# Kernel optimization log

Hardware: AMD Instinct MI355X
Metric: run time of the kernel (lower is better)

The kernel has to match this reference:

```python
import jax, jax.numpy as jnp
import numpy as np

B, CIN, COUT, H, W, K = 32, 256, 256, 64, 64, 3


def setup_inputs() -> dict:
    key = jax.random.key(0)
    k1, k2, k3 = jax.random.split(key, 3)
    x = jax.random.normal(k1, (B, CIN, H, W), dtype=jnp.float32)
    # kaiming_uniform_ with a=sqrt(5): bound = sqrt(6 / ((1 + a^2) * fan_in)) = sqrt(1/fan_in)
    fan_in = CIN * K * K
    bound = float(np.sqrt(1.0 / fan_in))
    weight = jax.random.uniform(k2, (COUT, CIN, K, K), dtype=jnp.float32,
                                minval=-bound, maxval=bound)
    bias = jax.random.normal(k3, (COUT,), dtype=jnp.float32)
    return {"x": x, "weight": weight, "bias": bias}


def reference(x, weight, bias):
    # CustomConvnd with kernel=3, stride=1, padding=1 (module doubles it, pad
    # helper splits around center -> 1 element each side, zero padding),
    # equivalent to a standard 2D cross-correlation like torch Conv2d.
    out = jax.lax.conv_general_dilated(
        x, weight,
        window_strides=(1, 1),
        padding=((1, 1), (1, 1)),
        dimension_numbers=("NCHW", "OIHW", "NCHW"),
    )
    return out + bias[None, :, None, None]
```

## Files before the change

### kernel.cpp

```cpp
#include <hip/hip_runtime.h>
#include <hip/hip_bf16.h>

typedef __attribute__((ext_vector_type(8))) short short8;
typedef __attribute__((ext_vector_type(16))) float floatx16;

#define BDIM 256

constexpr int kCIN = 256, kCOUT = 256, kH = 64, kW = 64;
constexpr int BK = 32;
constexpr int NCHUNK = kCIN / BK;
constexpr int ROWS = 2;
constexpr int XR = ROWS + 2, XC = 66, NPIX = XR * XC;
constexpr int HW = kH * kW;
constexpr int NSTEP = NCHUNK * 9;

constexpr int XS_PLANE = NPIX * 16;
constexpr int XS_BUF   = 4 * XS_PLANE;
constexpr int WS_PLANE = 256 * 16;
constexpr int WS_BUF   = 4 * WS_PLANE;

__device__ __forceinline__ unsigned short f2bf(float f) {
    unsigned u = __float_as_uint(f);
    u += 0x7fffu + ((u >> 16) & 1u);
    return (unsigned short)(u >> 16);
}

__global__ void wt_transform_kernel(const float* __restrict__ wsrc,
                                    unsigned short* __restrict__ wt2) {
    int idx = blockIdx.x * 256 + threadIdx.x;
    if (idx >= 9 * 256 * 256) return;
    int j  = idx & 7;
    int co = (idx >> 3) & 255;
    int g  = (idx >> 11) & 3;
    int chunk = (idx >> 13) & 7;
    int kk = idx >> 16;
    int ci = chunk * 32 + g * 8 + j;
    wt2[idx] = f2bf(wsrc[(co * 256 + ci) * 9 + kk]);
}

__global__ __launch_bounds__(BDIM, 2)
void conv3x3_mfma_kernel(const float* __restrict__ x,
                         const unsigned short* __restrict__ wt2,
                         const float* __restrict__ bias,
                         float* __restrict__ out) {
    __shared__ __align__(16) char xs[2 * XS_BUF];
    __shared__ __align__(16) char ws[2 * WS_BUF];

    const int bid = blockIdx.x;
    const int b  = bid >> 5;
    const int h0 = (bid & 31) * ROWS;

    const int tid = threadIdx.x;
    const int wv  = tid >> 6;
    const int l   = tid & 63;
    const int l31 = l & 31;
    const int hi2 = l >> 5;
    const int cog  = (wv & 1) * 128;
    const int wrow = wv >> 1;

    const float* xb = x + (size_t)b * kCIN * HW;

    floatx16 acc[4][2] = {};

    auto stageW = [&](int st) {
        int chunk = st / 9, kk = st - chunk * 9;
        char* wbuf = ws + (st & 1) * WS_BUF;
        const unsigned short* wp = wt2 + (size_t)(kk * 8 + chunk) * 8192;
        #pragma unroll
        for (int it = 0; it < 4; ++it) {
            int c = wv * 4 + it;
            int g = c >> 2;
            int row0 = (c & 3) * 64;
            const unsigned short* src = wp + (g * 256 + row0 + l) * 8;
            __builtin_amdgcn_global_load_lds(
                (const __attribute__((address_space(1))) unsigned int*)src,
                (__attribute__((address_space(3))) unsigned int*)
                    (wbuf + g * WS_PLANE + row0 * 16),
                16, 0, 0);
        }
    };

    auto stageX = [&](int chunk) {
        char* xbuf = xs + (chunk & 1) * XS_BUF;
        const int ci0 = chunk * BK;
        for (int t = tid; t < NPIX * 4; t += BDIM) {
            int g = t / NPIX;
            int rem = t - g * NPIX;
            int r = rem / XC;
            int c = rem - r * XC;
            int ih = h0 - 1 + r;
            int iw = c - 1;
            float v[8];
            if ((unsigned)ih < (unsigned)kH && (unsigned)iw < (unsigned)kW) {
                const float* p = xb + (size_t)(ci0 + g * 8) * HW + ih * kW + iw;
                #pragma unroll
                for (int j = 0; j < 8; ++j) v[j] = p[(size_t)j * HW];
            } else {
                #pragma unroll
                for (int j = 0; j < 8; ++j) v[j] = 0.f;
            }
            union { short8 s8; unsigned short u[8]; } pk;
            #pragma unroll
            for (int j = 0; j < 8; ++j) pk.u[j] = f2bf(v[j]);
            int pix = r * XC + c;
            *(short8*)(xbuf + g * XS_PLANE + pix * 16) = pk.s8;
        }
    };

    stageX(0);
    stageW(0);
    __syncthreads();

    int chunk = 0, kk = 0;
    #pragma unroll 1
    for (int t = 0; t < NSTEP; ++t) {
        if (t + 1 < NSTEP) stageW(t + 1);
        if (kk == 8 && chunk + 1 < NCHUNK) stageX(chunk + 1);

        const char* wbuf = ws + (t & 1) * WS_BUF;
        const char* xbuf = xs + (chunk & 1) * XS_BUF;
        const int kh = kk / 3, kwo = kk - kh * 3;
        const int r = wrow + kh;

        short8 a[2][4], bfr[2][2];
        #pragma unroll
        for (int s = 0; s < 2; ++s) {
            const int g = s * 2 + hi2;
            #pragma unroll
            for (int i = 0; i < 4; ++i) {
                int co = cog + i * 32 + l31;
                a[s][i] = *(const short8*)(wbuf + g * WS_PLANE + co * 16);
            }
            #pragma unroll
            for (int f = 0; f < 2; ++f) {
                int pix = r * XC + f * 32 + l31 + kwo;
                bfr[s][f] = *(const short8*)(xbuf + g * XS_PLANE + pix * 16);
            }
        }
        #pragma unroll
        for (int s = 0; s < 2; ++s)
            #pragma unroll
            for (int i = 0; i < 4; ++i)
                #pragma unroll
                for (int f = 0; f < 2; ++f)
                    acc[i][f] = __builtin_amdgcn_mfma_f32_32x32x16_bf16(
                        a[s][i], bfr[s][f], acc[i][f], 0, 0, 0);

        __syncthreads();

        kk++;
        if (kk == 9) { kk = 0; chunk++; }
    }

    float* op = out + (size_t)b * kCOUT * HW + (size_t)(h0 + wrow) * kW;
    #pragma unroll
    for (int i = 0; i < 4; ++i) {
        #pragma unroll
        for (int rg = 0; rg < 16; ++rg) {
            int co = cog + i * 32 + (rg & 3) + 8 * (rg >> 2) + 4 * hi2;
            float bv = bias[co];
            #pragma unroll
            for (int f = 0; f < 2; ++f) {
                op[(size_t)co * HW + f * 32 + l31] = acc[i][f][rg] + bv;
            }
        }
    }
}

extern "C" void kernel_launch(void* const* d_in, const int* in_sizes, int n_in,
                              void* d_out, int out_size, void* d_ws, size_t ws_size,
                              hipStream_t stream) {
    const float* x    = (const float*)d_in[0];
    const float* wsrc = (const float*)d_in[1];
    const float* bias = (const float*)d_in[2];
    float* out = (float*)d_out;
    unsigned short* wt2 = (unsigned short*)d_ws;

    hipLaunchKernelGGL(wt_transform_kernel, dim3((9 * 256 * 256 + 255) / 256),
                       dim3(256), 0, stream, wsrc, wt2);

    hipLaunchKernelGGL(conv3x3_mfma_kernel, dim3(32 * (kH / ROWS)), dim3(BDIM),
                       0, stream, x, wt2, bias, out);
}
```

Measured before the change: 180.8 us.

## Load conv weights straight into double-buffered registers and sync once per chunk

Weight fragments are no longer staged through LDS. Each wave now loads its A operands directly from global memory (L2-resident bf16 weights) into two register buffers that alternate across taps. This removes the per-tap __syncthreads, which is now needed only once per input-channel chunk. Staging of the next input chunk moves earlier (tap 2) so it can overlap more compute, and its loop is fully unrolled. In exchange it adds register pressure from the two A buffers and more global/L2 traffic per wave, and it relies on global load latency being hidden by the register double buffering.

```diff
diff --git a/kernel.cpp b/kernel.cpp
--- a/kernel.cpp
+++ b/kernel.cpp
@@ -16,8 +16,6 @@
 
 constexpr int XS_PLANE = NPIX * 16;
 constexpr int XS_BUF   = 4 * XS_PLANE;
-constexpr int WS_PLANE = 256 * 16;
-constexpr int WS_BUF   = 4 * WS_PLANE;
 
 __device__ __forceinline__ unsigned short f2bf(float f) {
     unsigned u = __float_as_uint(f);
@@ -44,7 +42,6 @@
                          const float* __restrict__ bias,
                          float* __restrict__ out) {
     __shared__ __align__(16) char xs[2 * XS_BUF];
-    __shared__ __align__(16) char ws[2 * WS_BUF];
 
     const int bid = blockIdx.x;
     const int b  = bid >> 5;
@@ -62,75 +59,60 @@
 
     floatx16 acc[4][2] = {};
 
-    auto stageW = [&](int st) {
-        int chunk = st / 9, kk = st - chunk * 9;
-        char* wbuf = ws + (st & 1) * WS_BUF;
+    auto loadA = [&](int t, short8 a[2][4]) {
+        int chunk = t / 9, kk = t - chunk * 9;
         const unsigned short* wp = wt2 + (size_t)(kk * 8 + chunk) * 8192;
         #pragma unroll
-        for (int it = 0; it < 4; ++it) {
-            int c = wv * 4 + it;
-            int g = c >> 2;
-            int row0 = (c & 3) * 64;
-            const unsigned short* src = wp + (g * 256 + row0 + l) * 8;
-            __builtin_amdgcn_global_load_lds(
-                (const __attribute__((address_space(1))) unsigned int*)src,
-                (__attribute__((address_space(3))) unsigned int*)
-                    (wbuf + g * WS_PLANE + row0 * 16),
-                16, 0, 0);
+        for (int s = 0; s < 2; ++s) {
+            const int g = s * 2 + hi2;
+            #pragma unroll
+            for (int i = 0; i < 4; ++i) {
+                int co = cog + i * 32 + l31;
+                a[s][i] = *(const short8*)(wp + (g * 256 + co) * 8);
+            }
         }
     };
 
     auto stageX = [&](int chunk) {
         char* xbuf = xs + (chunk & 1) * XS_BUF;
         const int ci0 = chunk * BK;
-        for (int t = tid; t < NPIX * 4; t += BDIM) {
-            int g = t / NPIX;
-            int rem = t - g * NPIX;
-            int r = rem / XC;
-            int c = rem - r * XC;
-            int ih = h0 - 1 + r;
-            int iw = c - 1;
-            float v[8];
-            if ((unsigned)ih < (unsigned)kH && (unsigned)iw < (unsigned)kW) {
-                const float* p = xb + (size_t)(ci0 + g * 8) * HW + ih * kW + iw;
+        #pragma unroll
+        for (int it = 0; it < 5; ++it) {
+            int t = tid + it * BDIM;
+            if (it < 4 || t < NPIX * 4) {
+                int g = t / NPIX;
+                int rem = t - g * NPIX;
+                int r = rem / XC;
+                int c = rem - r * XC;
+                int ih = h0 - 1 + r;
+                int iw = c - 1;
+                float v[8];
+                if ((unsigned)ih < (unsigned)kH && (unsigned)iw < (unsigned)kW) {
+                    const float* p = xb + (size_t)(ci0 + g * 8) * HW + ih * kW + iw;
+                    #pragma unroll
+                    for (int j = 0; j < 8; ++j) v[j] = p[(size_t)j * HW];
+                } else {
+                    #pragma unroll
+                    for (int j = 0; j < 8; ++j) v[j] = 0.f;
+                }
+                union { short8 s8; unsigned short u[8]; } pk;
                 #pragma unroll
-                for (int j = 0; j < 8; ++j) v[j] = p[(size_t)j * HW];
-            } else {
-                #pragma unroll
-                for (int j = 0; j < 8; ++j) v[j] = 0.f;
+                for (int j = 0; j < 8; ++j) pk.u[j] = f2bf(v[j]);
+                int pix = r * XC + c;
+                *(short8*)(xbuf + g * XS_PLANE + pix * 16) = pk.s8;
             }
-            union { short8 s8; unsigned short u[8]; } pk;
-            #pragma unroll
-            for (int j = 0; j < 8; ++j) pk.u[j] = f2bf(v[j]);
-            int pix = r * XC + c;
-            *(short8*)(xbuf + g * XS_PLANE + pix * 16) = pk.s8;
         }
     };
 
-    stageX(0);
-    stageW(0);
-    __syncthreads();
-
-    int chunk = 0, kk = 0;
-    #pragma unroll 1
-    for (int t = 0; t < NSTEP; ++t) {
-        if (t + 1 < NSTEP) stageW(t + 1);
-        if (kk == 8 && chunk + 1 < NCHUNK) stageX(chunk + 1);
-
-        const char* wbuf = ws + (t & 1) * WS_BUF;
+    auto tapCompute = [&](int t, short8 a[2][4]) {
+        int chunk = t / 9, kk = t - chunk * 9;
         const char* xbuf = xs + (chunk & 1) * XS_BUF;
         const int kh = kk / 3, kwo = kk - kh * 3;
         const int r = wrow + kh;
-
-        short8 a[2][4], bfr[2][2];
+        short8 bfr[2][2];
         #pragma unroll
         for (int s = 0; s < 2; ++s) {
             const int g = s * 2 + hi2;
-            #pragma unroll
-            for (int i = 0; i < 4; ++i) {
-                int co = cog + i * 32 + l31;
-                a[s][i] = *(const short8*)(wbuf + g * WS_PLANE + co * 16);
-            }
             #pragma unroll
             for (int f = 0; f < 2; ++f) {
                 int pix = r * XC + f * 32 + l31 + kwo;
@@ -145,11 +127,33 @@
                 for (int f = 0; f < 2; ++f)
                     acc[i][f] = __builtin_amdgcn_mfma_f32_32x32x16_bf16(
                         a[s][i], bfr[s][f], acc[i][f], 0, 0, 0);
+    };
 
-        __syncthreads();
+    auto postTap = [&](int t) {
+        int chunk = t / 9, kk = t - chunk * 9;
+        if (kk == 2 && chunk + 1 < NCHUNK) stageX(chunk + 1);
+        if (kk == 8 && t < NSTEP - 1) {
+            __builtin_amdgcn_sched_barrier(0);
+            asm volatile("s_waitcnt lgkmcnt(0)" ::: "memory");
+            __builtin_amdgcn_sched_barrier(0);
+            __builtin_amdgcn_s_barrier();
+            __builtin_amdgcn_sched_barrier(0);
+        }
+    };
 
-        kk++;
-        if (kk == 9) { kk = 0; chunk++; }
+    stageX(0);
+    short8 aA[2][4], aB[2][4];
+    loadA(0, aA);
+    __syncthreads();
+
+    #pragma unroll 1
+    for (int t = 0; t < NSTEP; t += 2) {
+        if (t + 1 < NSTEP) loadA(t + 1, aB);
+        tapCompute(t, aA);
+        postTap(t);
+        if (t + 2 < NSTEP) loadA(t + 2, aA);
+        tapCompute(t + 1, aB);
+        postTap(t + 1);
     }
 
     float* op = out + (size_t)b * kCOUT * HW + (size_t)(h0 + wrow) * kW;
```

New measurement: 163.3 us. 1.11x faster.
